# Performance work log

Measured on AMD Instinct MI355X. Metric: run time of the kernel, lower is better.

Reference implementation:

```python
import jax, jax.numpy as jnp
import numpy as np
from jax import lax

B, T, H, W, C = 2, 16, 64, 64, 64
KT, K = 3, 3


def kernel_to_freq_3d(kernel, T, H, W):
    # kernel: (C, k_t, k_h, k_w) -> (C, T, H, W) complex freq response
    Cc, k_t, k_h, k_w = kernel.shape
    t_idx = (jnp.arange(k_t) - k_t // 2) % T
    h_idx = (jnp.arange(k_h) - k_h // 2) % H
    w_idx = (jnp.arange(k_w) - k_w // 2) % W
    tt, th, tw = jnp.meshgrid(t_idx, h_idx, w_idx, indexing='ij')
    padded = jnp.zeros((Cc, T, H, W), dtype=kernel.dtype).at[:, tt, th, tw].set(kernel)
    return jnp.fft.fftn(padded, axes=(1, 2, 3))


def mamba_op(left, right):
    a1, b1 = left
    a2, b2 = right
    return (a1 * a2, a2 * b1 + b2)


def setup_inputs() -> dict:
    key = jax.random.key(0)
    ks = jax.random.split(key, 8)
    fan_in = KT * K * K
    x = jax.random.normal(ks[0], (B, T, H, W, C), dtype=jnp.float32)
    A_kernel = jax.random.normal(ks[1], (C, KT, K, K), dtype=jnp.float32) / np.sqrt(fan_in)
    B_kernel = jax.random.normal(ks[2], (C, KT, K, K), dtype=jnp.float32) / np.sqrt(fan_in)
    forget_bias = jnp.full((C,), 2.0, dtype=jnp.float32)
    forget_scale = jnp.full((C,), 0.01, dtype=jnp.float32)
    input_bias = jnp.zeros((C,), dtype=jnp.float32)
    input_scale = jnp.full((C,), 0.01, dtype=jnp.float32)
    delta_W = jax.random.normal(ks[3], (C, C), dtype=jnp.float32) / np.sqrt(C)
    delta_b = jnp.zeros((C,), dtype=jnp.float32)
    return {"x": x, "A_kernel": A_kernel, "B_kernel": B_kernel,
            "forget_bias": forget_bias, "forget_scale": forget_scale,
            "input_bias": input_bias, "input_scale": input_scale,
            "delta_W": delta_W, "delta_b": delta_b}


def reference(x, A_kernel, B_kernel, forget_bias, forget_scale,
              input_bias, input_scale, delta_W, delta_b):
    Bb, Tt, Hh, Ww, Cc = x.shape
    # freq-domain kernels: (C,T,H,W) -> (T,1,H,W,C) for broadcasting over batch
    A_f = kernel_to_freq_3d(A_kernel, Tt, Hh, Ww).transpose(1, 2, 3, 0)[:, None]
    B_f = kernel_to_freq_3d(B_kernel, Tt, Hh, Ww).transpose(1, 2, 3, 0)[:, None]
    # input-dependent gates (real, elementwise per channel)
    forget_gate = jax.nn.sigmoid(forget_bias + forget_scale * x)
    input_gate = jax.nn.sigmoid(input_bias + input_scale * x)
    delta = jax.nn.softplus(jnp.einsum('bthwc,cd->bthwd', x, delta_W) + delta_b)
    x_f = jnp.fft.fftn(x, axes=(1, 2, 3))  # complex (B,T,H,W,C)
    # move time axis to front for the scan: (T,B,H,W,C)
    a_seq = forget_gate.transpose(1, 0, 2, 3, 4) * A_f
    b_seq = (input_gate.transpose(1, 0, 2, 3, 4)
             * delta.transpose(1, 0, 2, 3, 4)
             * B_f * x_f.transpose(1, 0, 2, 3, 4))
    _, h_all_f = lax.associative_scan(mamba_op, (a_seq, b_seq), axis=0)
    h_f = h_all_f.transpose(1, 0, 2, 3, 4)
    h = jnp.fft.ifftn(h_f, axes=(1, 2, 3)).real
    return h.astype(x.dtype)
```

## Files before the change

kernel.cpp:

```cpp
#include <hip/hip_runtime.h>
#include <math.h>

#define Bb 2
#define Tt 16
#define Hh 64
#define Ww 64
#define Cc 64
#define ST_ (Hh*Ww*Cc)
#define SB_ (Tt*Hh*Ww*Cc)

#define TWO_PI 6.2831853071795864769f

typedef __attribute__((ext_vector_type(8))) short bf16x8;
typedef __attribute__((ext_vector_type(4))) float f32x4;

#define BUF_A    0u
#define BUF_B    8388608u
#define OFF_PRE  16777216u
#define OFF_TWF  16779264u
#define OFF_THF  16783360u
#define OFF_THI  16791552u
#define OFF_TWI  16799744u

__device__ __forceinline__ float2 cmul(float2 a, float2 b) {
    return make_float2(fmaf(a.x, b.x, -a.y * b.y), fmaf(a.x, b.y, a.y * b.x));
}
__device__ __forceinline__ float2 cadd(float2 a, float2 b) { return make_float2(a.x + b.x, a.y + b.y); }
__device__ __forceinline__ float2 csub(float2 a, float2 b) { return make_float2(a.x - b.x, a.y - b.y); }

__device__ __forceinline__ unsigned bfpack(float2 f) {
    unsigned r = __float_as_uint(f.x);
    unsigned i = __float_as_uint(f.y);
    r = (r + 0x7fffu + ((r >> 16) & 1u)) >> 16;
    i = (i + 0x7fffu + ((i >> 16) & 1u)) >> 16;
    return r | (i << 16);
}
__device__ __forceinline__ float2 bfunpack(unsigned u) {
    return make_float2(__uint_as_float(u << 16), __uint_as_float(u & 0xffff0000u));
}

template <int S>
__device__ __forceinline__ void fft4(float2& a, float2& b, float2& c, float2& d) {
    float2 t0 = cadd(a, c), t1 = csub(a, c);
    float2 t2 = cadd(b, d), t3 = csub(b, d);
    a = cadd(t0, t2);
    c = csub(t0, t2);
    b = make_float2(t1.x - (float)S * t3.y, t1.y + (float)S * t3.x);
    d = make_float2(t1.x + (float)S * t3.y, t1.y - (float)S * t3.x);
}

template <int S>
__device__ __forceinline__ void fft16(float2 v[16]) {
    const float CS[10] = {1.f, 0.92387953f, 0.70710678f, 0.38268343f, 0.f,
                          -0.38268343f, -0.70710678f, -0.92387953f, -1.f, -0.92387953f};
    const float SN[10] = {0.f, 0.38268343f, 0.70710678f, 0.92387953f, 1.f,
                          0.92387953f, 0.70710678f, 0.38268343f, 0.f, -0.38268343f};
    float2 A[4][4];
#pragma unroll
    for (int j = 0; j < 4; ++j) {
        A[j][0] = v[j]; A[j][1] = v[4 + j]; A[j][2] = v[8 + j]; A[j][3] = v[12 + j];
        fft4<S>(A[j][0], A[j][1], A[j][2], A[j][3]);
#pragma unroll
        for (int k0 = 0; k0 < 4; ++k0) {
            int m = j * k0;
            float2 tw = make_float2(CS[m], (float)S * SN[m]);
            A[j][k0] = cmul(A[j][k0], tw);
        }
    }
#pragma unroll
    for (int k0 = 0; k0 < 4; ++k0) {
        fft4<S>(A[0][k0], A[1][k0], A[2][k0], A[3][k0]);
        v[k0] = A[0][k0]; v[k0 + 4] = A[1][k0]; v[k0 + 8] = A[2][k0]; v[k0 + 12] = A[3][k0];
    }
}

__global__ __launch_bounds__(256) void k_setup(const float* __restrict__ dW,
                                               unsigned* __restrict__ ws) {
    int j = blockIdx.x * 256 + threadIdx.x;
    if (j < 2048) {
        int p2 = j & 3, lane = (j >> 2) & 63, ka = (j >> 8) & 1, nt = j >> 9;
        int kb = ka * 32 + (lane >> 4) * 8 + 2 * p2;
        int ccol = (lane & 15) + 16 * nt;
        ws[OFF_PRE + j] = bfpack(make_float2(dW[kb * 64 + ccol], dW[(kb + 1) * 64 + ccol]));
        return;
    }
    int idx, table;
    if (j < 6144)       { idx = j - 2048;  table = 0; }
    else if (j < 14336) { idx = j - 6144;  table = 1; }
    else if (j < 22528) { idx = j - 14336; table = 2; }
    else                { idx = j - 22528; table = 3; }
    int p = idx & 3;
    int lane = (idx >> 2) & 63;
    int m = lane & 15, q = lane >> 4;
    int ka, r, reim;
    if (table == 0)      { ka = (idx >> 8) & 1; r = (idx >> 9) & 3;  reim = (idx >> 11) & 1; }
    else if (table == 3) { ka = (idx >> 8) & 3; r = (idx >> 10) & 3; reim = 0; }
    else                 { ka = (idx >> 8) & 3; r = (idx >> 10) & 3; reim = (idx >> 12) & 1; }
    int wp = r * 16 + m;
    int k0 = ka * 32 + q * 8 + 2 * p;
    float val[2];
#pragma unroll
    for (int dk = 0; dk < 2; ++dk) {
        int k = k0 + dk;
        float v;
        if (table == 0) {
            int a = (wp * k) & 63;
            float sn, cs; sincosf(TWO_PI * (float)a * (1.0f / 64.0f), &sn, &cs);
            v = (reim == 0) ? cs : -sn;
        } else {
            int h = k >> 1;
            int a = (wp * h) & 63;
            float sn, cs; sincosf(TWO_PI * (float)a * (1.0f / 64.0f), &sn, &cs);
            bool even = (k & 1) == 0;
            if (table == 1) {
                v = (reim == 0) ? (even ? cs : sn) : (even ? -sn : cs);
            } else if (table == 2) {
                v = (reim == 0) ? (even ? cs : -sn) : (even ? sn : cs);
                v *= (1.0f / 64.0f);
            } else {
                v = (even ? cs : -sn) * (1.0f / 64.0f);
            }
        }
        val[dk] = v;
    }
    unsigned base = (table == 0) ? OFF_TWF : (table == 1) ? OFF_THF
                  : (table == 2) ? OFF_THI : OFF_TWI;
    ws[base + idx] = bfpack(make_float2(val[0], val[1]));
}

__global__ __launch_bounds__(256) void k_dft_w_fwd(const float* __restrict__ x,
                                                   unsigned* __restrict__ X1,
                                                   const uint4* __restrict__ T) {
    __shared__ unsigned zw[64 * 66];
    int tid = threadIdx.x;
    int s = blockIdx.x;
    const float* src = x + (size_t)s * 4096;
    for (int idx = tid; idx < 2048; idx += 256) {
        int i = idx >> 6, c = idx & 63;
        zw[c * 66 + i] = bfpack(make_float2(src[i * 128 + c], src[i * 128 + 64 + c]));
    }
    __syncthreads();

    int r = tid >> 6, lane = tid & 63;
    int m = lane & 15, q = lane >> 4;
    union U48 { uint4 u4; uint2 u2[2]; unsigned u[4]; bf16x8 v8; };
    U48 Are[2], Aim[2], Bf;
#pragma unroll
    for (int ka = 0; ka < 2; ++ka) {
        Are[ka].u4 = T[((0 * 4 + r) * 2 + ka) * 64 + lane];
        Aim[ka].u4 = T[((1 * 4 + r) * 2 + ka) * 64 + lane];
    }
    f32x4 ar[4], ai[4];
#pragma unroll
    for (int nt = 0; nt < 4; ++nt) { ar[nt] = (f32x4){0.f,0.f,0.f,0.f}; ai[nt] = (f32x4){0.f,0.f,0.f,0.f}; }
#pragma unroll
    for (int nt = 0; nt < 4; ++nt) {
        int cc = m + 16 * nt;
#pragma unroll
        for (int ka = 0; ka < 2; ++ka) {
            int i0 = ka * 16 + q * 4;
            Bf.u2[0] = *(const uint2*)&zw[cc * 66 + i0];
            Bf.u2[1] = *(const uint2*)&zw[cc * 66 + i0 + 2];
            ar[nt] = __builtin_amdgcn_mfma_f32_16x16x32_bf16(Are[ka].v8, Bf.v8, ar[nt], 0, 0, 0);
            ai[nt] = __builtin_amdgcn_mfma_f32_16x16x32_bf16(Aim[ka].v8, Bf.v8, ai[nt], 0, 0, 0);
        }
    }
    int bt = s >> 6, h = s & 63;
    size_t ob = (size_t)bt * 262144 + (size_t)h * 64;
#pragma unroll
    for (int nt = 0; nt < 4; ++nt) {
        int cc = m + 16 * nt;
#pragma unroll
        for (int reg = 0; reg < 4; ++reg) {
            int wp = r * 16 + q * 4 + reg;
            X1[ob + (size_t)wp * 4096 + cc] = bfpack(make_float2(ar[nt][reg], ai[nt][reg]));
        }
    }
}

__global__ __launch_bounds__(256) void k_dft_h_fwd(const unsigned* __restrict__ X1,
                                                   unsigned* __restrict__ X2,
                                                   const uint4* __restrict__ T) {
    __shared__ unsigned zs[64 * 66];
    int tid = threadIdx.x;
    int s = blockIdx.x;
    const unsigned* src = X1 + (size_t)s * 4096;
    for (int i = tid; i < 4096; i += 256) {
        int h = i >> 6, c = i & 63;
        zs[c * 66 + h] = src[i];
    }
    __syncthreads();

    int r = tid >> 6, lane = tid & 63;
    int m = lane & 15, q = lane >> 4;
    union U48 { uint4 u4; uint2 u2[2]; unsigned u[4]; bf16x8 v8; };
    U48 Are[4], Aim[4], Bf;
#pragma unroll
    for (int ka = 0; ka < 4; ++ka) {
        Are[ka].u4 = T[((0 * 4 + r) * 4 + ka) * 64 + lane];
        Aim[ka].u4 = T[((1 * 4 + r) * 4 + ka) * 64 + lane];
    }
    f32x4 ar[4], ai[4];
#pragma unroll
    for (int nt = 0; nt < 4; ++nt) { ar[nt] = (f32x4){0.f,0.f,0.f,0.f}; ai[nt] = (f32x4){0.f,0.f,0.f,0.f}; }
#pragma unroll
    for (int nt = 0; nt < 4; ++nt) {
        int cc = m + 16 * nt;
#pragma unroll
        for (int ka = 0; ka < 4; ++ka) {
            int h0 = ka * 16 + q * 4;
            Bf.u2[0] = *(const uint2*)&zs[cc * 66 + h0];
            Bf.u2[1] = *(const uint2*)&zs[cc * 66 + h0 + 2];
            ar[nt] = __builtin_amdgcn_mfma_f32_16x16x32_bf16(Are[ka].v8, Bf.v8, ar[nt], 0, 0, 0);
            ai[nt] = __builtin_amdgcn_mfma_f32_16x16x32_bf16(Aim[ka].v8, Bf.v8, ai[nt], 0, 0, 0);
        }
    }
    int b = s >> 10, t = (s >> 6) & 15, w = s & 63;
    size_t ob = (size_t)b * 4194304 + (size_t)w * 1024 + (size_t)t * 64;
#pragma unroll
    for (int nt = 0; nt < 4; ++nt) {
        int cc = m + 16 * nt;
#pragma unroll
        for (int reg = 0; reg < 4; ++reg) {
            int hp = r * 16 + q * 4 + reg;
            X2[ob + (size_t)hp * 65536 + cc] = bfpack(make_float2(ar[nt][reg], ai[nt][reg]));
        }
    }
}

__global__ __launch_bounds__(256) void k_dft_h_inv(const unsigned* __restrict__ X3,
                                                   unsigned* __restrict__ X4,
                                                   const uint4* __restrict__ T) {
    __shared__ unsigned zs[64 * 66];
    int tid = threadIdx.x;
    int s = blockIdx.x;
    const unsigned* src = X3 + (size_t)s * 4096;
    for (int i = tid; i < 4096; i += 256) {
        int h = i >> 6, c = i & 63;
        zs[c * 66 + h] = src[i];
    }
    __syncthreads();

    int r = tid >> 6, lane = tid & 63;
    int m = lane & 15, q = lane >> 4;
    union U48 { uint4 u4; uint2 u2[2]; unsigned u[4]; bf16x8 v8; };
    U48 Are[4], Aim[4], Bf;
#pragma unroll
    for (int ka = 0; ka < 4; ++ka) {
        Are[ka].u4 = T[((0 * 4 + r) * 4 + ka) * 64 + lane];
        Aim[ka].u4 = T[((1 * 4 + r) * 4 + ka) * 64 + lane];
    }
    f32x4 ar[4], ai[4];
#pragma unroll
    for (int nt = 0; nt < 4; ++nt) { ar[nt] = (f32x4){0.f,0.f,0.f,0.f}; ai[nt] = (f32x4){0.f,0.f,0.f,0.f}; }
#pragma unroll
    for (int nt = 0; nt < 4; ++nt) {
        int cc = m + 16 * nt;
#pragma unroll
        for (int ka = 0; ka < 4; ++ka) {
            int h0 = ka * 16 + q * 4;
            Bf.u2[0] = *(const uint2*)&zs[cc * 66 + h0];
            Bf.u2[1] = *(const uint2*)&zs[cc * 66 + h0 + 2];
            ar[nt] = __builtin_amdgcn_mfma_f32_16x16x32_bf16(Are[ka].v8, Bf.v8, ar[nt], 0, 0, 0);
            ai[nt] = __builtin_amdgcn_mfma_f32_16x16x32_bf16(Aim[ka].v8, Bf.v8, ai[nt], 0, 0, 0);
        }
    }
    int bt = s >> 6, w = s & 63;
    size_t ob = (size_t)bt * 262144 + (size_t)w * 64;
#pragma unroll
    for (int nt = 0; nt < 4; ++nt) {
        int cc = m + 16 * nt;
#pragma unroll
        for (int reg = 0; reg < 4; ++reg) {
            int hp = r * 16 + q * 4 + reg;
            X4[ob + (size_t)hp * 4096 + cc] = bfpack(make_float2(ar[nt][reg], ai[nt][reg]));
        }
    }
}

__global__ __launch_bounds__(256) void k_dft_w_inv(const unsigned* __restrict__ X4,
                                                   float* __restrict__ out,
                                                   const uint4* __restrict__ T) {
    __shared__ unsigned zs[64 * 66];
    int tid = threadIdx.x;
    int s = blockIdx.x;
    const unsigned* src = X4 + (size_t)s * 4096;
    for (int i = tid; i < 4096; i += 256) {
        int w = i >> 6, c = i & 63;
        zs[c * 66 + w] = src[i];
    }
    __syncthreads();

    int r = tid >> 6, lane = tid & 63;
    int m = lane & 15, q = lane >> 4;
    union U48 { uint4 u4; uint2 u2[2]; unsigned u[4]; bf16x8 v8; };
    U48 Are[4], Bf;
#pragma unroll
    for (int ka = 0; ka < 4; ++ka)
        Are[ka].u4 = T[(r * 4 + ka) * 64 + lane];
    f32x4 ar[4];
#pragma unroll
    for (int nt = 0; nt < 4; ++nt) ar[nt] = (f32x4){0.f,0.f,0.f,0.f};
#pragma unroll
    for (int nt = 0; nt < 4; ++nt) {
        int cc = m + 16 * nt;
#pragma unroll
        for (int ka = 0; ka < 4; ++ka) {
            int w0 = ka * 16 + q * 4;
            Bf.u2[0] = *(const uint2*)&zs[cc * 66 + w0];
            Bf.u2[1] = *(const uint2*)&zs[cc * 66 + w0 + 2];
            ar[nt] = __builtin_amdgcn_mfma_f32_16x16x32_bf16(Are[ka].v8, Bf.v8, ar[nt], 0, 0, 0);
        }
    }
    float* dst = out + (size_t)s * 4096;
#pragma unroll
    for (int nt = 0; nt < 4; ++nt) {
        int cc = m + 16 * nt;
#pragma unroll
        for (int reg = 0; reg < 4; ++reg) {
            int wp = r * 16 + q * 4 + reg;
            dst[wp * 64 + cc] = ar[nt][reg];
        }
    }
}

__global__ __launch_bounds__(256) void k_mid(
    const float* __restrict__ x, const unsigned* __restrict__ X2,
    unsigned* __restrict__ X3,
    const float* __restrict__ Ak, const float* __restrict__ Bk,
    const float* __restrict__ fb, const float* __restrict__ fs,
    const float* __restrict__ ib, const float* __restrict__ isc_,
    const uint4* __restrict__ pre, const float* __restrict__ db) {
    const float CT[16] = {1.f, 0.9238795f, 0.7071068f, 0.3826834f, 0.f, -0.3826834f,
                          -0.7071068f, -0.9238795f, -1.f, -0.9238795f, -0.7071068f,
                          -0.3826834f, 0.f, 0.3826834f, 0.7071068f, 0.9238795f};
    const float SN[16] = {0.f, 0.3826834f, 0.7071068f, 0.9238795f, 1.f, 0.9238795f,
                          0.7071068f, 0.3826834f, 0.f, -0.3826834f, -0.7071068f,
                          -0.9238795f, -1.f, -0.9238795f, -0.7071068f, -0.3826834f};
    __shared__ float Akl[1728], Bkl[1728];
    __shared__ __align__(16) float xs[4][16 * 68 + 4];

    int tid = threadIdx.x;
    int g = tid >> 6, lane = tid & 63;
    int c = lane;
    int site = blockIdx.x * 4 + g;
    int b = site >> 12, hw = site & 4095;
    int h = hw >> 6, w = hw & 63;
    size_t base = (size_t)b * SB_ + (size_t)hw * 64;

    for (int i = tid; i < 1728; i += 256) { Akl[i] = Ak[i]; Bkl[i] = Bk[i]; }

    float xv[16];
    float2 v[16];
    const unsigned* src2 = X2 + (size_t)site * 1024;
#pragma unroll
    for (int t = 0; t < 16; ++t) {
        xv[t] = x[base + (size_t)t * ST_ + c];
        v[t] = bfunpack(src2[t * 64 + c]);
    }
#pragma unroll
    for (int t = 0; t < 16; ++t) xs[g][t * 68 + c] = xv[t];
    __syncthreads();

    int m = lane & 15, q = lane >> 4;
    bf16x8 Afrag[2];
#pragma unroll
    for (int ka = 0; ka < 2; ++ka) {
        int d0 = ka * 32 + q * 8;
        const float* p = &xs[g][m * 68 + d0];
        float4 f0 = *(const float4*)p;
        float4 f1 = *(const float4*)(p + 4);
        union { bf16x8 v8; unsigned u[4]; } U;
        U.u[0] = bfpack(make_float2(f0.x, f0.y));
        U.u[1] = bfpack(make_float2(f0.z, f0.w));
        U.u[2] = bfpack(make_float2(f1.x, f1.y));
        U.u[3] = bfpack(make_float2(f1.z, f1.w));
        Afrag[ka] = U.v8;
    }
#pragma unroll
    for (int nt = 0; nt < 4; ++nt) {
        int ccol = m + 16 * nt;
        float dbn = db[ccol];
        f32x4 acc = {dbn, dbn, dbn, dbn};
#pragma unroll
        for (int ka = 0; ka < 2; ++ka) {
            union { bf16x8 v8; uint4 u4; } Ub;
            Ub.u4 = pre[(nt * 2 + ka) * 64 + lane];
            acc = __builtin_amdgcn_mfma_f32_16x16x32_bf16(Afrag[ka], Ub.v8, acc, 0, 0, 0);
        }
#pragma unroll
        for (int reg = 0; reg < 4; ++reg)
            xs[g][(q * 4 + reg) * 68 + ccol] = acc[reg];
    }

    float sh, ch; sincosf(TWO_PI * (float)h / 64.0f, &sh, &ch);
    float sw, cw; sincosf(TWO_PI * (float)w / 64.0f, &sw, &cw);
    float2 eh[3] = { make_float2(ch, sh), make_float2(1.f, 0.f), make_float2(ch, -sh) };
    float2 ew[3] = { make_float2(cw, sw), make_float2(1.f, 0.f), make_float2(cw, -sw) };
    float2 GA[3], GB[3];
#pragma unroll
    for (int kt = 0; kt < 3; ++kt) { GA[kt] = make_float2(0.f, 0.f); GB[kt] = make_float2(0.f, 0.f); }
#pragma unroll
    for (int kh = 0; kh < 3; ++kh) {
#pragma unroll
        for (int kw = 0; kw < 3; ++kw) {
            float2 e = cmul(eh[kh], ew[kw]);
#pragma unroll
            for (int kt = 0; kt < 3; ++kt) {
                float ka = Akl[c * 27 + kt * 9 + kh * 3 + kw];
                float kb = Bkl[c * 27 + kt * 9 + kh * 3 + kw];
                GA[kt].x = fmaf(ka, e.x, GA[kt].x);
                GA[kt].y = fmaf(ka, e.y, GA[kt].y);
                GB[kt].x = fmaf(kb, e.x, GB[kt].x);
                GB[kt].y = fmaf(kb, e.y, GB[kt].y);
            }
        }
    }
    float fbc = fb[c], fsc = fs[c], ibc = ib[c], iscv = isc_[c];

    fft16<-1>(v);
    __syncthreads();

    float delta_raw[16];
#pragma unroll
    for (int t = 0; t < 16; ++t) delta_raw[t] = xs[g][t * 68 + c];

    float2 hv = make_float2(0.f, 0.f);
#pragma unroll
    for (int t = 0; t < 16; ++t) {
        float ct = CT[t], st = SN[t];
        float2 Af, Bf;
        Af.x = GA[1].x + ct * (GA[0].x + GA[2].x) - st * (GA[0].y - GA[2].y);
        Af.y = GA[1].y + ct * (GA[0].y + GA[2].y) + st * (GA[0].x - GA[2].x);
        Bf.x = GB[1].x + ct * (GB[0].x + GB[2].x) - st * (GB[0].y - GB[2].y);
        Bf.y = GB[1].y + ct * (GB[0].y + GB[2].y) + st * (GB[0].x - GB[2].x);

        float xc = xv[t];
        float fg  = __builtin_amdgcn_rcpf(1.f + __expf(-(fbc + fsc * xc)));
        float igv = __builtin_amdgcn_rcpf(1.f + __expf(-(ibc + iscv * xc)));
        float dot = delta_raw[t];
        float delta = (dot > 20.f) ? dot : __logf(1.f + __expf(dot));

        float sR = igv * delta;
        float2 bbv;
        bbv.x = sR * (Bf.x * v[t].x - Bf.y * v[t].y);
        bbv.y = sR * (Bf.x * v[t].y + Bf.y * v[t].x);
        float2 av = make_float2(fg * Af.x, fg * Af.y);
        float2 nh;
        nh.x = av.x * hv.x - av.y * hv.y + bbv.x;
        nh.y = av.x * hv.y + av.y * hv.x + bbv.y;
        hv = nh;
        v[t] = hv;
    }

    fft16<1>(v);

    size_t ob = (size_t)b * 4194304 + (size_t)w * 4096 + (size_t)h * 64 + c;
#pragma unroll
    for (int t = 0; t < 16; ++t) {
        float2 o = make_float2(v[t].x * 0.0625f, v[t].y * 0.0625f);
        X3[ob + (size_t)t * 262144] = bfpack(o);
    }
}

extern "C" void kernel_launch(void* const* d_in, const int* in_sizes, int n_in,
                              void* d_out, int out_size, void* d_ws, size_t ws_size,
                              hipStream_t stream) {
    const float* x   = (const float*)d_in[0];
    const float* Ak  = (const float*)d_in[1];
    const float* Bk  = (const float*)d_in[2];
    const float* fb  = (const float*)d_in[3];
    const float* fs  = (const float*)d_in[4];
    const float* ib  = (const float*)d_in[5];
    const float* is_ = (const float*)d_in[6];
    const float* dW  = (const float*)d_in[7];
    const float* db  = (const float*)d_in[8];
    float* out = (float*)d_out;
    unsigned* ws = (unsigned*)d_ws;
    unsigned* A = ws + BUF_A;
    unsigned* B = ws + BUF_B;

    k_setup<<<104, 256, 0, stream>>>(dW, ws);
    k_dft_w_fwd<<<Bb * Tt * Hh, 256, 0, stream>>>(x, A, (const uint4*)(ws + OFF_TWF));
    k_dft_h_fwd<<<Bb * Tt * Ww, 256, 0, stream>>>(A, B, (const uint4*)(ws + OFF_THF));
    k_mid<<<(Bb * Hh * Ww) / 4, 256, 0, stream>>>(x, B, A, Ak, Bk, fb, fs, ib, is_,
                                                  (const uint4*)(ws + OFF_PRE), db);
    k_dft_h_inv<<<Bb * Tt * Ww, 256, 0, stream>>>(A, B, (const uint4*)(ws + OFF_THI));
    k_dft_w_inv<<<Bb * Tt * Hh, 256, 0, stream>>>(B, out, (const uint4*)(ws + OFF_TWI));
}
```

Baseline: 175.2 us.

## Process two slices per block in DFT kernels with double-buffered LDS staging

```diff
diff --git a/kernel.cpp b/kernel.cpp
--- a/kernel.cpp
+++ b/kernel.cpp
@@ -37,6 +37,14 @@
 }
 __device__ __forceinline__ float2 bfunpack(unsigned u) {
     return make_float2(__uint_as_float(u << 16), __uint_as_float(u & 0xffff0000u));
+}
+
+union U48 { uint4 u4; uint2 u2[2]; unsigned u[4]; bf16x8 v8; };
+
+__device__ __forceinline__ void wg_barrier_lds() {
+    asm volatile("s_waitcnt lgkmcnt(0)" ::: "memory");
+    __builtin_amdgcn_s_barrier();
+    __builtin_amdgcn_sched_barrier(0);
 }
 
 template <int S>
@@ -128,28 +136,83 @@
     ws[base + idx] = bfpack(make_float2(val[0], val[1]));
 }
 
-__global__ __launch_bounds__(256) void k_dft_w_fwd(const float* __restrict__ x,
-                                                   unsigned* __restrict__ X1,
-                                                   const uint4* __restrict__ T) {
-    __shared__ unsigned zw[64 * 66];
-    int tid = threadIdx.x;
-    int s = blockIdx.x;
-    const float* src = x + (size_t)s * 4096;
-    for (int idx = tid; idx < 2048; idx += 256) {
-        int i = idx >> 6, c = idx & 63;
-        zw[c * 66 + i] = bfpack(make_float2(src[i * 128 + c], src[i * 128 + 64 + c]));
-    }
-    __syncthreads();
-
-    int r = tid >> 6, lane = tid & 63;
-    int m = lane & 15, q = lane >> 4;
-    union U48 { uint4 u4; uint2 u2[2]; unsigned u[4]; bf16x8 v8; };
-    U48 Are[2], Aim[2], Bf;
-#pragma unroll
-    for (int ka = 0; ka < 2; ++ka) {
-        Are[ka].u4 = T[((0 * 4 + r) * 2 + ka) * 64 + lane];
-        Aim[ka].u4 = T[((1 * 4 + r) * 2 + ka) * 64 + lane];
-    }
+__device__ __forceinline__ void stage_load(const unsigned* __restrict__ src, int tid,
+                                           uint4 rr[4]) {
+#pragma unroll
+    for (int i = 0; i < 4; ++i)
+        rr[i] = *(const uint4*)&src[i * 1024 + tid * 4];
+}
+__device__ __forceinline__ void stage_write(unsigned* zs, int tid, const uint4 rr[4]) {
+#pragma unroll
+    for (int i = 0; i < 4; ++i) {
+        int lin = i * 1024 + tid * 4;
+        int h = lin >> 6, c0 = lin & 63;
+        unsigned* p = &zs[c0 * 66 + h];
+        p[0]   = rr[i].x;
+        p[66]  = rr[i].y;
+        p[132] = rr[i].z;
+        p[198] = rr[i].w;
+    }
+}
+
+__device__ __forceinline__ void dft_cpx(const unsigned* zs, const U48 Are[4],
+                                        const U48 Aim[4], int m, int q, int r,
+                                        unsigned* __restrict__ dst, size_t ob,
+                                        int hstride) {
+    f32x4 ar[4], ai[4];
+#pragma unroll
+    for (int nt = 0; nt < 4; ++nt) { ar[nt] = (f32x4){0.f,0.f,0.f,0.f}; ai[nt] = (f32x4){0.f,0.f,0.f,0.f}; }
+#pragma unroll
+    for (int nt = 0; nt < 4; ++nt) {
+        int cc = m + 16 * nt;
+#pragma unroll
+        for (int ka = 0; ka < 4; ++ka) {
+            int h0 = ka * 16 + q * 4;
+            U48 Bf;
+            Bf.u2[0] = *(const uint2*)&zs[cc * 66 + h0];
+            Bf.u2[1] = *(const uint2*)&zs[cc * 66 + h0 + 2];
+            ar[nt] = __builtin_amdgcn_mfma_f32_16x16x32_bf16(Are[ka].v8, Bf.v8, ar[nt], 0, 0, 0);
+            ai[nt] = __builtin_amdgcn_mfma_f32_16x16x32_bf16(Aim[ka].v8, Bf.v8, ai[nt], 0, 0, 0);
+        }
+    }
+#pragma unroll
+    for (int nt = 0; nt < 4; ++nt) {
+        int cc = m + 16 * nt;
+#pragma unroll
+        for (int reg = 0; reg < 4; ++reg) {
+            int hp = r * 16 + q * 4 + reg;
+            dst[ob + (size_t)hp * hstride + cc] = bfpack(make_float2(ar[nt][reg], ai[nt][reg]));
+        }
+    }
+}
+
+__device__ __forceinline__ void stage_load_w(const float* __restrict__ src, int tid,
+                                             float4 fa[2][2]) {
+#pragma unroll
+    for (int it = 0; it < 2; ++it) {
+        int id = it * 256 + tid;
+        int p = id >> 4, c0 = (id & 15) * 4;
+        fa[it][0] = *(const float4*)&src[(2 * p) * 64 + c0];
+        fa[it][1] = *(const float4*)&src[(2 * p + 1) * 64 + c0];
+    }
+}
+__device__ __forceinline__ void stage_write_w(unsigned* zw, int tid, const float4 fa[2][2]) {
+#pragma unroll
+    for (int it = 0; it < 2; ++it) {
+        int id = it * 256 + tid;
+        int p = id >> 4, c0 = (id & 15) * 4;
+        const float4 a = fa[it][0];
+        const float4 b = fa[it][1];
+        zw[(c0 + 0) * 66 + p] = bfpack(make_float2(a.x, b.x));
+        zw[(c0 + 1) * 66 + p] = bfpack(make_float2(a.y, b.y));
+        zw[(c0 + 2) * 66 + p] = bfpack(make_float2(a.z, b.z));
+        zw[(c0 + 3) * 66 + p] = bfpack(make_float2(a.w, b.w));
+    }
+}
+
+__device__ __forceinline__ void dft_w_fwd_compute(const unsigned* zw, const U48 Are[2],
+                                                  const U48 Aim[2], int m, int q, int r,
+                                                  unsigned* __restrict__ X1, int s) {
     f32x4 ar[4], ai[4];
 #pragma unroll
     for (int nt = 0; nt < 4; ++nt) { ar[nt] = (f32x4){0.f,0.f,0.f,0.f}; ai[nt] = (f32x4){0.f,0.f,0.f,0.f}; }
@@ -159,6 +222,7 @@
 #pragma unroll
         for (int ka = 0; ka < 2; ++ka) {
             int i0 = ka * 16 + q * 4;
+            U48 Bf;
             Bf.u2[0] = *(const uint2*)&zw[cc * 66 + i0];
             Bf.u2[1] = *(const uint2*)&zw[cc * 66 + i0 + 2];
             ar[nt] = __builtin_amdgcn_mfma_f32_16x16x32_bf16(Are[ka].v8, Bf.v8, ar[nt], 0, 0, 0);
@@ -178,102 +242,127 @@
     }
 }
 
+__global__ __launch_bounds__(256) void k_dft_w_fwd(const float* __restrict__ x,
+                                                   unsigned* __restrict__ X1,
+                                                   const uint4* __restrict__ T) {
+    __shared__ unsigned zw[2][64 * 66];
+    int tid = threadIdx.x;
+    int s0 = blockIdx.x * 2;
+    int r = tid >> 6, lane = tid & 63;
+    int m = lane & 15, q = lane >> 4;
+    U48 Are[2], Aim[2];
+#pragma unroll
+    for (int ka = 0; ka < 2; ++ka) {
+        Are[ka].u4 = T[((0 * 4 + r) * 2 + ka) * 64 + lane];
+        Aim[ka].u4 = T[((1 * 4 + r) * 2 + ka) * 64 + lane];
+    }
+    float4 fa[2][2], fb[2][2];
+    stage_load_w(x + (size_t)s0 * 4096, tid, fa);
+    stage_write_w(zw[0], tid, fa);
+    stage_load_w(x + (size_t)(s0 + 1) * 4096, tid, fb);
+    wg_barrier_lds();
+    dft_w_fwd_compute(zw[0], Are, Aim, m, q, r, X1, s0);
+    stage_write_w(zw[1], tid, fb);
+    wg_barrier_lds();
+    dft_w_fwd_compute(zw[1], Are, Aim, m, q, r, X1, s0 + 1);
+}
+
 __global__ __launch_bounds__(256) void k_dft_h_fwd(const unsigned* __restrict__ X1,
                                                    unsigned* __restrict__ X2,
                                                    const uint4* __restrict__ T) {
-    __shared__ unsigned zs[64 * 66];
+    __shared__ unsigned zs[2][64 * 66];
     int tid = threadIdx.x;
-    int s = blockIdx.x;
-    const unsigned* src = X1 + (size_t)s * 4096;
-    for (int i = tid; i < 4096; i += 256) {
-        int h = i >> 6, c = i & 63;
-        zs[c * 66 + h] = src[i];
-    }
-    __syncthreads();
-
+    int s0 = blockIdx.x * 2;
     int r = tid >> 6, lane = tid & 63;
     int m = lane & 15, q = lane >> 4;
-    union U48 { uint4 u4; uint2 u2[2]; unsigned u[4]; bf16x8 v8; };
-    U48 Are[4], Aim[4], Bf;
+    U48 Are[4], Aim[4];
 #pragma unroll
     for (int ka = 0; ka < 4; ++ka) {
         Are[ka].u4 = T[((0 * 4 + r) * 4 + ka) * 64 + lane];
         Aim[ka].u4 = T[((1 * 4 + r) * 4 + ka) * 64 + lane];
     }
-    f32x4 ar[4], ai[4];
-#pragma unroll
-    for (int nt = 0; nt < 4; ++nt) { ar[nt] = (f32x4){0.f,0.f,0.f,0.f}; ai[nt] = (f32x4){0.f,0.f,0.f,0.f}; }
-#pragma unroll
-    for (int nt = 0; nt < 4; ++nt) {
-        int cc = m + 16 * nt;
-#pragma unroll
-        for (int ka = 0; ka < 4; ++ka) {
-            int h0 = ka * 16 + q * 4;
-            Bf.u2[0] = *(const uint2*)&zs[cc * 66 + h0];
-            Bf.u2[1] = *(const uint2*)&zs[cc * 66 + h0 + 2];
-            ar[nt] = __builtin_amdgcn_mfma_f32_16x16x32_bf16(Are[ka].v8, Bf.v8, ar[nt], 0, 0, 0);
-            ai[nt] = __builtin_amdgcn_mfma_f32_16x16x32_bf16(Aim[ka].v8, Bf.v8, ai[nt], 0, 0, 0);
-        }
-    }
-    int b = s >> 10, t = (s >> 6) & 15, w = s & 63;
-    size_t ob = (size_t)b * 4194304 + (size_t)w * 1024 + (size_t)t * 64;
-#pragma unroll
-    for (int nt = 0; nt < 4; ++nt) {
-        int cc = m + 16 * nt;
-#pragma unroll
-        for (int reg = 0; reg < 4; ++reg) {
-            int hp = r * 16 + q * 4 + reg;
-            X2[ob + (size_t)hp * 65536 + cc] = bfpack(make_float2(ar[nt][reg], ai[nt][reg]));
-        }
+    uint4 ra[4], rb[4];
+    stage_load(X1 + (size_t)s0 * 4096, tid, ra);
+    stage_write(zs[0], tid, ra);
+    stage_load(X1 + (size_t)(s0 + 1) * 4096, tid, rb);
+    wg_barrier_lds();
+    {
+        int s = s0;
+        int b = s >> 10, t = (s >> 6) & 15, w = s & 63;
+        size_t ob = (size_t)b * 4194304 + (size_t)w * 1024 + (size_t)t * 64;
+        dft_cpx(zs[0], Are, Aim, m, q, r, X2, ob, 65536);
+    }
+    stage_write(zs[1], tid, rb);
+    wg_barrier_lds();
+    {
+        int s = s0 + 1;
+        int b = s >> 10, t = (s >> 6) & 15, w = s & 63;
+        size_t ob = (size_t)b * 4194304 + (size_t)w * 1024 + (size_t)t * 64;
+        dft_cpx(zs[1], Are, Aim, m, q, r, X2, ob, 65536);
     }
 }
 
 __global__ __launch_bounds__(256) void k_dft_h_inv(const unsigned* __restrict__ X3,
                                                    unsigned* __restrict__ X4,
                                                    const uint4* __restrict__ T) {
-    __shared__ unsigned zs[64 * 66];
+    __shared__ unsigned zs[2][64 * 66];
     int tid = threadIdx.x;
-    int s = blockIdx.x;
-    const unsigned* src = X3 + (size_t)s * 4096;
-    for (int i = tid; i < 4096; i += 256) {
-        int h = i >> 6, c = i & 63;
-        zs[c * 66 + h] = src[i];
-    }
-    __syncthreads();
-
+    int s0 = blockIdx.x * 2;
     int r = tid >> 6, lane = tid & 63;
     int m = lane & 15, q = lane >> 4;
-    union U48 { uint4 u4; uint2 u2[2]; unsigned u[4]; bf16x8 v8; };
-    U48 Are[4], Aim[4], Bf;
+    U48 Are[4], Aim[4];
 #pragma unroll
     for (int ka = 0; ka < 4; ++ka) {
         Are[ka].u4 = T[((0 * 4 + r) * 4 + ka) * 64 + lane];
         Aim[ka].u4 = T[((1 * 4 + r) * 4 + ka) * 64 + lane];
     }
-    f32x4 ar[4], ai[4];
-#pragma unroll
-    for (int nt = 0; nt < 4; ++nt) { ar[nt] = (f32x4){0.f,0.f,0.f,0.f}; ai[nt] = (f32x4){0.f,0.f,0.f,0.f}; }
+    uint4 ra[4], rb[4];
+    stage_load(X3 + (size_t)s0 * 4096, tid, ra);
+    stage_write(zs[0], tid, ra);
+    stage_load(X3 + (size_t)(s0 + 1) * 4096, tid, rb);
+    wg_barrier_lds();
+    {
+        int s = s0;
+        int bt = s >> 6, w = s & 63;
+        size_t ob = (size_t)bt * 262144 + (size_t)w * 64;
+        dft_cpx(zs[0], Are, Aim, m, q, r, X4, ob, 4096);
+    }
+    stage_write(zs[1], tid, rb);
+    wg_barrier_lds();
+    {
+        int s = s0 + 1;
+        int bt = s >> 6, w = s & 63;
+        size_t ob = (size_t)bt * 262144 + (size_t)w * 64;
+        dft_cpx(zs[1], Are, Aim, m, q, r, X4, ob, 4096);
+    }
+}
+
+__device__ __forceinline__ void dft_w_inv_compute(const unsigned* zs, const U48 Are[4],
+                                                  int m, int q, int r,
+                                                  float* __restrict__ out, int s) {
+    f32x4 ar[4];
+#pragma unroll
+    for (int nt = 0; nt < 4; ++nt) ar[nt] = (f32x4){0.f,0.f,0.f,0.f};
 #pragma unroll
     for (int nt = 0; nt < 4; ++nt) {
         int cc = m + 16 * nt;
 #pragma unroll
         for (int ka = 0; ka < 4; ++ka) {
-            int h0 = ka * 16 + q * 4;
-            Bf.u2[0] = *(const uint2*)&zs[cc * 66 + h0];
-            Bf.u2[1] = *(const uint2*)&zs[cc * 66 + h0 + 2];
+            int w0 = ka * 16 + q * 4;
+            U48 Bf;
+            Bf.u2[0] = *(const uint2*)&zs[cc * 66 + w0];
+            Bf.u2[1] = *(const uint2*)&zs[cc * 66 + w0 + 2];
             ar[nt] = __builtin_amdgcn_mfma_f32_16x16x32_bf16(Are[ka].v8, Bf.v8, ar[nt], 0, 0, 0);
-            ai[nt] = __builtin_amdgcn_mfma_f32_16x16x32_bf16(Aim[ka].v8, Bf.v8, ai[nt], 0, 0, 0);
-        }
-    }
-    int bt = s >> 6, w = s & 63;
-    size_t ob = (size_t)bt * 262144 + (size_t)w * 64;
+        }
+    }
+    float* dst = out + (size_t)s * 4096;
 #pragma unroll
     for (int nt = 0; nt < 4; ++nt) {
         int cc = m + 16 * nt;
 #pragma unroll
         for (int reg = 0; reg < 4; ++reg) {
-            int hp = r * 16 + q * 4 + reg;
-            X4[ob + (size_t)hp * 4096 + cc] = bfpack(make_float2(ar[nt][reg], ai[nt][reg]));
+            int wp = r * 16 + q * 4 + reg;
+            dst[wp * 64 + cc] = ar[nt][reg];
         }
     }
 }
@@ -281,47 +370,24 @@
 __global__ __launch_bounds__(256) void k_dft_w_inv(const unsigned* __restrict__ X4,
                                                    float* __restrict__ out,
                                                    const uint4* __restrict__ T) {
-    __shared__ unsigned zs[64 * 66];
+    __shared__ unsigned zs[2][64 * 66];
     int tid = threadIdx.x;
-    int s = blockIdx.x;
-    const unsigned* src = X4 + (size_t)s * 4096;
-    for (int i = tid; i < 4096; i += 256) {
-        int w = i >> 6, c = i & 63;
-        zs[c * 66 + w] = src[i];
-    }
-    __syncthreads();
-
+    int s0 = blockIdx.x * 2;
     int r = tid >> 6, lane = tid & 63;
     int m = lane & 15, q = lane >> 4;
-    union U48 { uint4 u4; uint2 u2[2]; unsigned u[4]; bf16x8 v8; };
-    U48 Are[4], Bf;
+    U48 Are[4];
 #pragma unroll
     for (int ka = 0; ka < 4; ++ka)
         Are[ka].u4 = T[(r * 4 + ka) * 64 + lane];
-    f32x4 ar[4];
-#pragma unroll
-    for (int nt = 0; nt < 4; ++nt) ar[nt] = (f32x4){0.f,0.f,0.f,0.f};
-#pragma unroll
-    for (int nt = 0; nt < 4; ++nt) {
-        int cc = m + 16 * nt;
-#pragma unroll
-        for (int ka = 0; ka < 4; ++ka) {
-            int w0 = ka * 16 + q * 4;
-            Bf.u2[0] = *(const uint2*)&zs[cc * 66 + w0];
-            Bf.u2[1] = *(const uint2*)&zs[cc * 66 + w0 + 2];
-            ar[nt] = __builtin_amdgcn_mfma_f32_16x16x32_bf16(Are[ka].v8, Bf.v8, ar[nt], 0, 0, 0);
-        }
-    }
-    float* dst = out + (size_t)s * 4096;
-#pragma unroll
-    for (int nt = 0; nt < 4; ++nt) {
-        int cc = m + 16 * nt;
-#pragma unroll
-        for (int reg = 0; reg < 4; ++reg) {
-            int wp = r * 16 + q * 4 + reg;
-            dst[wp * 64 + cc] = ar[nt][reg];
-        }
-    }
+    uint4 ra[4], rb[4];
+    stage_load(X4 + (size_t)s0 * 4096, tid, ra);
+    stage_write(zs[0], tid, ra);
+    stage_load(X4 + (size_t)(s0 + 1) * 4096, tid, rb);
+    wg_barrier_lds();
+    dft_w_inv_compute(zs[0], Are, m, q, r, out, s0);
+    stage_write(zs[1], tid, rb);
+    wg_barrier_lds();
+    dft_w_inv_compute(zs[1], Are, m, q, r, out, s0 + 1);
 }
 
 __global__ __launch_bounds__(256) void k_mid(
@@ -481,10 +547,10 @@
     unsigned* B = ws + BUF_B;
 
     k_setup<<<104, 256, 0, stream>>>(dW, ws);
-    k_dft_w_fwd<<<Bb * Tt * Hh, 256, 0, stream>>>(x, A, (const uint4*)(ws + OFF_TWF));
-    k_dft_h_fwd<<<Bb * Tt * Ww, 256, 0, stream>>>(A, B, (const uint4*)(ws + OFF_THF));
+    k_dft_w_fwd<<<Bb * Tt * Hh / 2, 256, 0, stream>>>(x, A, (const uint4*)(ws + OFF_TWF));
+    k_dft_h_fwd<<<Bb * Tt * Ww / 2, 256, 0, stream>>>(A, B, (const uint4*)(ws + OFF_THF));
     k_mid<<<(Bb * Hh * Ww) / 4, 256, 0, stream>>>(x, B, A, Ak, Bk, fb, fs, ib, is_,
                                                   (const uint4*)(ws + OFF_PRE), db);
-    k_dft_h_inv<<<Bb * Tt * Ww, 256, 0, stream>>>(A, B, (const uint4*)(ws + OFF_THI));
-    k_dft_w_inv<<<Bb * Tt * Hh, 256, 0, stream>>>(B, out, (const uint4*)(ws + OFF_TWI));
-}
+    k_dft_h_inv<<<Bb * Tt * Ww / 2, 256, 0, stream>>>(A, B, (const uint4*)(ws + OFF_THI));
+    k_dft_w_inv<<<Bb * Tt * Hh / 2, 256, 0, stream>>>(B, out, (const uint4*)(ws + OFF_TWI));
+}
```

Measured after the change: 170.3 us. 2.8% less time.
